# Performance work log

Hardware: AMD Instinct MI355X
Metric: run time of the kernel (lower is better)

The kernel has to match this reference:

```python
import jax, jax.numpy as jnp
import numpy as np

N_EMBD = 768
N_HEAD = 12
B, T = 2, 2048


def setup_inputs() -> dict:
    key = jax.random.key(0)
    ks = jax.random.split(key, 8)
    C = N_EMBD
    s = 0.02
    return {
        "x": jax.random.normal(ks[0], (B, T, C), jnp.float32),
        "ln1_g": jnp.ones((C,), jnp.float32),
        "ln1_b": jnp.zeros((C,), jnp.float32),
        "w_attn": jax.random.normal(ks[1], (C, 3 * C), jnp.float32) * s,
        "b_attn": jnp.zeros((3 * C,), jnp.float32),
        "w_attn_proj": jax.random.normal(ks[2], (C, C), jnp.float32) * s,
        "b_attn_proj": jnp.zeros((C,), jnp.float32),
        "ln2_g": jnp.ones((C,), jnp.float32),
        "ln2_b": jnp.zeros((C,), jnp.float32),
        "w_fc": jax.random.normal(ks[3], (C, 4 * C), jnp.float32) * s,
        "b_fc": jnp.zeros((4 * C,), jnp.float32),
        "w_mlp_proj": jax.random.normal(ks[4], (4 * C, C), jnp.float32) * s,
        "b_mlp_proj": jnp.zeros((C,), jnp.float32),
    }


def _layernorm(x, g, b, eps=1e-5):
    mu = jnp.mean(x, axis=-1, keepdims=True)
    var = jnp.mean(jnp.square(x - mu), axis=-1, keepdims=True)
    return (x - mu) * jax.lax.rsqrt(var + eps) * g + b


def _new_gelu(x):
    c = np.sqrt(2.0 / np.pi).astype(np.float32)
    return 0.5 * x * (1.0 + jnp.tanh(c * (x + 0.044715 * x * x * x)))


def _block(x, ln1_g, ln1_b, w_attn, b_attn, w_attn_proj, b_attn_proj,
           ln2_g, ln2_b, w_fc, b_fc, w_mlp_proj, b_mlp_proj):
    Bx, Tx, C = x.shape
    hd = C // N_HEAD
    h = _layernorm(x, ln1_g, ln1_b)
    qkv = h @ w_attn + b_attn  # [B,T,3C]
    q, k, v = jnp.split(qkv, 3, axis=-1)
    # [B,H,T,hd]
    q = q.reshape(Bx, Tx, N_HEAD, hd).transpose(0, 2, 1, 3)
    k = k.reshape(Bx, Tx, N_HEAD, hd).transpose(0, 2, 1, 3)
    v = v.reshape(Bx, Tx, N_HEAD, hd).transpose(0, 2, 1, 3)
    att = jnp.einsum('bhqd,bhkd->bhqk', q, k) * (1.0 / np.sqrt(hd))
    causal = jnp.tril(jnp.ones((Tx, Tx), bool))
    att = jnp.where(causal[None, None], att, -jnp.inf)
    att = jax.nn.softmax(att, axis=-1)
    y = jnp.einsum('bhqk,bhkd->bhqd', att, v)
    y = y.transpose(0, 2, 1, 3).reshape(Bx, Tx, C)
    x = x + y @ w_attn_proj + b_attn_proj
    h2 = _layernorm(x, ln2_g, ln2_b)
    x = x + _new_gelu(h2 @ w_fc + b_fc) @ w_mlp_proj + b_mlp_proj
    return x


def reference(x, ln1_g, ln1_b, w_attn, b_attn, w_attn_proj, b_attn_proj,
              ln2_g, ln2_b, w_fc, b_fc, w_mlp_proj, b_mlp_proj):
    return _block(x, ln1_g, ln1_b, w_attn, b_attn, w_attn_proj, b_attn_proj,
                  ln2_g, ln2_b, w_fc, b_fc, w_mlp_proj, b_mlp_proj)
```

## Files before the change

### kernel.cpp

```cpp
#include <hip/hip_runtime.h>
#include <hip/hip_bf16.h>
#include <math.h>

#define N_EMBD 768
#define N_HEAD 12
#define BATCH  2
#define SEQ    2048
#define ROWS   (BATCH*SEQ)
#define C3     (3*N_EMBD)

typedef __bf16 bf16;
typedef __attribute__((ext_vector_type(8))) __bf16 bf16x8;
typedef __attribute__((ext_vector_type(4))) float f32x4;

__device__ __forceinline__ void async16(const bf16* g, bf16* l) {
    __builtin_amdgcn_global_load_lds(
        (const __attribute__((address_space(1))) uint32_t*)g,
        (__attribute__((address_space(3))) uint32_t*)l, 16, 0, 0);
}

__global__ __launch_bounds__(256) void k_transpose_all(
    const float* __restrict__ w0, bf16* __restrict__ o0,
    const float* __restrict__ w1, bf16* __restrict__ o1,
    const float* __restrict__ w2, bf16* __restrict__ o2,
    const float* __restrict__ w3, bf16* __restrict__ o3)
{
    __shared__ bf16 tile[32][33];
    int bid = blockIdx.x;
    const float* in; bf16* out; int K, N, local;
    if      (bid < 1728) { in = w0; out = o0; K = 768;  N = 2304; local = bid; }
    else if (bid < 2304) { in = w1; out = o1; K = 768;  N = 768;  local = bid - 1728; }
    else if (bid < 4608) { in = w2; out = o2; K = 768;  N = 3072; local = bid - 2304; }
    else                 { in = w3; out = o3; K = 3072; N = 768;  local = bid - 4608; }
    int nt = N / 32;
    int n0 = (local % nt) * 32, k0 = (local / nt) * 32;
    int tc = threadIdx.x & 31, tr = threadIdx.x >> 5;
    #pragma unroll
    for (int i = 0; i < 4; i++) {
        int r = tr + i * 8;
        tile[r][tc] = (bf16)in[(size_t)(k0 + r) * N + n0 + tc];
    }
    __syncthreads();
    #pragma unroll
    for (int i = 0; i < 4; i++) {
        int r = tr + i * 8;
        out[(size_t)(n0 + r) * K + k0 + tc] = tile[tc][r];
    }
}

__global__ __launch_bounds__(256) void k_vtrans(
    const bf16* __restrict__ qkv, bf16* __restrict__ vt)
{
    __shared__ bf16 tile[32][33];
    int tt = blockIdx.x;
    int bh = blockIdx.y;
    int dt = blockIdx.z;
    int b = bh / N_HEAD, h = bh % N_HEAD;
    int tc = threadIdx.x & 31, tr = threadIdx.x >> 5;
    #pragma unroll
    for (int i = 0; i < 4; i++) {
        int r = tr + i * 8;
        tile[r][tc] = qkv[(size_t)(b * SEQ + tt * 32 + r) * C3 + 2 * N_EMBD + h * 64 + dt * 32 + tc];
    }
    __syncthreads();
    #pragma unroll
    for (int i = 0; i < 4; i++) {
        int r = tr + i * 8;
        vt[(size_t)(bh * 64 + dt * 32 + r) * SEQ + tt * 32 + tc] = tile[tc][r];
    }
}

__global__ __launch_bounds__(256) void k_layernorm(
    const float* __restrict__ x, const float* __restrict__ g,
    const float* __restrict__ b, bf16* __restrict__ out)
{
    int wave = threadIdx.x >> 6, lane = threadIdx.x & 63;
    int row = blockIdx.x * 4 + wave;
    const float4* xr = (const float4*)(x + (size_t)row * N_EMBD);
    const float4* g4 = (const float4*)g;
    const float4* b4 = (const float4*)b;
    float4 v[3];
    float s = 0.f, sq = 0.f;
    #pragma unroll
    for (int i = 0; i < 3; i++) {
        v[i] = xr[lane + 64 * i];
        s  += v[i].x + v[i].y + v[i].z + v[i].w;
        sq += v[i].x * v[i].x + v[i].y * v[i].y + v[i].z * v[i].z + v[i].w * v[i].w;
    }
    #pragma unroll
    for (int off = 32; off > 0; off >>= 1) {
        s  += __shfl_xor(s, off);
        sq += __shfl_xor(sq, off);
    }
    float mu  = s * (1.f / N_EMBD);
    float var = sq * (1.f / N_EMBD) - mu * mu;
    float rs  = rsqrtf(var + 1e-5f);
    bf16* orow = out + (size_t)row * N_EMBD;
    #pragma unroll
    for (int i = 0; i < 3; i++) {
        float4 gv = g4[lane + 64 * i], bv = b4[lane + 64 * i];
        union { ushort4 u4; bf16 e[4]; } pk;
        pk.e[0] = (bf16)((v[i].x - mu) * rs * gv.x + bv.x);
        pk.e[1] = (bf16)((v[i].y - mu) * rs * gv.y + bv.y);
        pk.e[2] = (bf16)((v[i].z - mu) * rs * gv.z + bv.z);
        pk.e[3] = (bf16)((v[i].w - mu) * rs * gv.w + bv.w);
        *(ushort4*)&orow[(lane + 64 * i) * 4] = pk.u4;
    }
}

template<int BN, int ACT, bool RES, bool OUT_BF16>
__global__ __launch_bounds__(256) void k_gemm(
    const bf16* __restrict__ A, const bf16* __restrict__ Bt,
    const float* __restrict__ bias, const float* __restrict__ res,
    void* __restrict__ outp, int M, int N, int K)
{
    constexpr int WC  = BN / 64;
    constexpr int WR  = 4 / WC;
    constexpr int RPW = 128 / WR;
    constexpr int MI  = RPW / 16;
    __shared__ __align__(16) bf16 As[128 * 32];
    __shared__ __align__(16) bf16 Bs[BN * 32];
    int n0 = blockIdx.x * BN, m0 = blockIdx.y * 128;
    int t = threadIdx.x;
    int lane = t & 63, wave = t >> 6;
    int wr = wave / WC, wc = wave % WC;
    int quad = lane >> 4, l16 = lane & 15;

    f32x4 acc[MI][4];
    #pragma unroll
    for (int i = 0; i < MI; i++)
        #pragma unroll
        for (int j = 0; j < 4; j++) acc[i][j] = (f32x4){0.f, 0.f, 0.f, 0.f};

    int sr = t >> 2;
    int sc = t & 3;
    int gsw = ((sc ^ ((sr ^ (sr >> 2)) & 3))) * 8;
    int rsw = (quad ^ ((l16 ^ (l16 >> 2)) & 3)) * 8;

    for (int k0 = 0; k0 < K; k0 += 32) {
        __syncthreads();
        #pragma unroll
        for (int p = 0; p < 2; p++) {
            int r = sr + p * 64;
            async16(&A[(size_t)(m0 + r) * K + k0 + gsw], &As[r * 32 + sc * 8]);
        }
        #pragma unroll
        for (int p = 0; p < BN / 64; p++) {
            int r = sr + p * 64;
            async16(&Bt[(size_t)(n0 + r) * K + k0 + gsw], &Bs[r * 32 + sc * 8]);
        }
        __syncthreads();
        bf16x8 af[MI], bfv[4];
        #pragma unroll
        for (int i = 0; i < MI; i++)
            af[i]  = *(bf16x8*)&As[(wr * RPW + i * 16 + l16) * 32 + rsw];
        #pragma unroll
        for (int j = 0; j < 4; j++)
            bfv[j] = *(bf16x8*)&Bs[(wc * 64 + j * 16 + l16) * 32 + rsw];
        #pragma unroll
        for (int i = 0; i < MI; i++)
            #pragma unroll
            for (int j = 0; j < 4; j++)
                acc[i][j] = __builtin_amdgcn_mfma_f32_16x16x32_bf16(af[i], bfv[j], acc[i][j], 0, 0, 0);
    }

    float* outf = (float*)outp;
    bf16*  outb = (bf16*)outp;
    #pragma unroll
    for (int i = 0; i < MI; i++) {
        #pragma unroll
        for (int j = 0; j < 4; j++) {
            int col = n0 + wc * 64 + j * 16 + l16;
            float bv = bias[col];
            #pragma unroll
            for (int r = 0; r < 4; r++) {
                int row = m0 + wr * RPW + i * 16 + quad * 4 + r;
                float v = acc[i][j][r] + bv;
                if (ACT == 1) {
                    float z = 0.7978845608f * (v + 0.044715f * v * v * v);
                    v = v / (1.f + __expf(-2.f * z));
                }
                if (RES) v += res[(size_t)row * N + col];
                if (OUT_BF16) outb[(size_t)row * N + col] = (bf16)v;
                else          outf[(size_t)row * N + col] = v;
            }
        }
    }
}

#define PS_S 72
__global__ __launch_bounds__(256) void k_flash(
    const bf16* __restrict__ qkv, const bf16* __restrict__ vt, bf16* __restrict__ y)
{
    __shared__ __align__(16) bf16 Ks[2][64 * 64];
    __shared__ __align__(16) bf16 VTl[2][64 * 64];
    __shared__ __align__(16) bf16 Ps[4][16 * PS_S];
    int bid = blockIdx.x;
    int hi = bid >> 8;
    int lo = bid & 255;
    int g  = lo >> 3;
    int e  = lo & 7;
    int bh = hi * 8 + e;
    int qt;
    if      (hi == 0) qt = g;
    else if (hi == 1) qt = (g + 16) & 31;
    else              qt = (g < 16) ? (30 - 2 * g) : (63 - 2 * g);
    int b = bh / N_HEAD, h = bh % N_HEAD;
    int t = threadIdx.x, lane = t & 63, wave = t >> 6;
    int quad = lane >> 4, l16 = lane & 15;
    int qbase = qt * 64 + wave * 16;

    bf16x8 qa[2];
    {
        const bf16* qrow = qkv + (size_t)(b * SEQ + qbase + l16) * C3 + h * 64;
        #pragma unroll
        for (int kh = 0; kh < 2; kh++) {
            union { uint4 u4; bf16 e8[8]; bf16x8 vv; } uq;
            uq.u4 = *(const uint4*)&qrow[quad * 8 + kh * 32];
            #pragma unroll
            for (int j = 0; j < 8; j++) uq.e8[j] = (bf16)((float)uq.e8[j] * 0.125f);
            qa[kh] = uq.vv;
        }
    }
    float l_part[4] = {0.f, 0.f, 0.f, 0.f};
    f32x4 o[4];
    #pragma unroll
    for (int j = 0; j < 4; j++) o[j] = (f32x4){0.f, 0.f, 0.f, 0.f};

    int sr = t >> 3;
    int sc = t & 7;
    int gsw = (sc ^ (sr & 7)) * 8;

    const bf16* kg = qkv + (size_t)b * SEQ * C3 + N_EMBD + h * 64;
    const bf16* vg = vt + (size_t)bh * 64 * SEQ;

    auto stage = [&](int tile, int bufi) {
        int k0 = tile * 64;
        #pragma unroll
        for (int p = 0; p < 2; p++) {
            int rr = sr + 32 * p;
            async16(&kg[(size_t)(k0 + rr) * C3 + gsw],  &Ks[bufi][rr * 64 + sc * 8]);
            async16(&vg[(size_t)rr * SEQ + k0 + gsw], &VTl[bufi][rr * 64 + sc * 8]);
        }
    };

    int ntiles = qt + 1;
    stage(0, 0);

    for (int tt = 0; tt < ntiles; tt++) {
        int bufi = tt & 1;
        int k0 = tt * 64;
        __syncthreads();
        if (tt + 1 < ntiles) stage(tt + 1, bufi ^ 1);

        f32x4 s[4];
        #pragma unroll
        for (int nt = 0; nt < 4; nt++) {
            bf16x8 b0 = *(bf16x8*)&Ks[bufi][(nt * 16 + l16) * 64 + (((quad    ) ^ (l16 & 7)) * 8)];
            bf16x8 b1 = *(bf16x8*)&Ks[bufi][(nt * 16 + l16) * 64 + (((quad + 4) ^ (l16 & 7)) * 8)];
            f32x4 z = (f32x4){0.f, 0.f, 0.f, 0.f};
            z = __builtin_amdgcn_mfma_f32_16x16x32_bf16(qa[0], b0, z, 0, 0, 0);
            z = __builtin_amdgcn_mfma_f32_16x16x32_bf16(qa[1], b1, z, 0, 0, 0);
            s[nt] = z;
        }
        bool diag = (tt == qt);
        float p[4][4];
        #pragma unroll
        for (int nt = 0; nt < 4; nt++) {
            int key = k0 + nt * 16 + l16;
            #pragma unroll
            for (int r = 0; r < 4; r++) {
                float pv = __expf(s[nt][r]);
                if (diag && key > qbase + quad * 4 + r) pv = 0.f;
                p[nt][r] = pv;
                l_part[r] += pv;
            }
        }
        #pragma unroll
        for (int nt = 0; nt < 4; nt++)
            #pragma unroll
            for (int r = 0; r < 4; r++)
                Ps[wave][(quad * 4 + r) * PS_S + nt * 16 + l16] = (bf16)p[nt][r];
        bf16x8 pa[2];
        #pragma unroll
        for (int kt = 0; kt < 2; kt++)
            pa[kt] = *(bf16x8*)&Ps[wave][l16 * PS_S + kt * 32 + quad * 8];
        #pragma unroll
        for (int jt = 0; jt < 4; jt++) {
            int d = jt * 16 + l16;
            #pragma unroll
            for (int kt = 0; kt < 2; kt++) {
                bf16x8 vb = *(bf16x8*)&VTl[bufi][d * 64 + (((quad + 4 * kt) ^ (l16 & 7)) * 8)];
                o[jt] = __builtin_amdgcn_mfma_f32_16x16x32_bf16(pa[kt], vb, o[jt], 0, 0, 0);
            }
        }
    }
    #pragma unroll
    for (int r = 0; r < 4; r++) {
        #pragma unroll
        for (int off = 8; off > 0; off >>= 1) l_part[r] += __shfl_xor(l_part[r], off);
    }
    #pragma unroll
    for (int jt = 0; jt < 4; jt++)
        #pragma unroll
        for (int r = 0; r < 4; r++) {
            int q = qbase + quad * 4 + r;
            y[(size_t)(b * SEQ + q) * N_EMBD + h * 64 + jt * 16 + l16] =
                (bf16)(o[jt][r] / l_part[r]);
        }
}

extern "C" void kernel_launch(void* const* d_in, const int* in_sizes, int n_in,
                              void* d_out, int out_size, void* d_ws, size_t ws_size,
                              hipStream_t stream) {
    const float* x           = (const float*)d_in[0];
    const float* ln1_g       = (const float*)d_in[1];
    const float* ln1_b       = (const float*)d_in[2];
    const float* w_attn      = (const float*)d_in[3];
    const float* b_attn      = (const float*)d_in[4];
    const float* w_attn_proj = (const float*)d_in[5];
    const float* b_attn_proj = (const float*)d_in[6];
    const float* ln2_g       = (const float*)d_in[7];
    const float* ln2_b       = (const float*)d_in[8];
    const float* w_fc        = (const float*)d_in[9];
    const float* b_fc        = (const float*)d_in[10];
    const float* w_mlp_proj  = (const float*)d_in[11];
    const float* b_mlp_proj  = (const float*)d_in[12];

    char* ws = (char*)d_ws;
    size_t off = 0;
    auto alloc = [&](size_t n) -> void* {
        off = (off + 255) & ~(size_t)255;
        void* p = ws + off;
        off += n;
        return p;
    };
    bf16* wqkvT  = (bf16*)alloc((size_t)C3 * N_EMBD * 2);
    bf16* wprojT = (bf16*)alloc((size_t)N_EMBD * N_EMBD * 2);
    bf16* wfcT   = (bf16*)alloc((size_t)4 * N_EMBD * N_EMBD * 2);
    bf16* wmlpT  = (bf16*)alloc((size_t)N_EMBD * 4 * N_EMBD * 2);
    bf16* hbuf   = (bf16*)alloc((size_t)ROWS * N_EMBD * 2);
    float* x2    = (float*)alloc((size_t)ROWS * N_EMBD * 4);
    bf16* yb     = (bf16*)alloc((size_t)ROWS * N_EMBD * 2);
    bf16* vtb    = (bf16*)alloc((size_t)BATCH * N_HEAD * 64 * SEQ * 2);
    bf16* big    = (bf16*)alloc((size_t)ROWS * 4 * N_EMBD * 2);
    bf16* qkvb   = big;
    bf16* actb   = big;

    k_transpose_all<<<6912, 256, 0, stream>>>(w_attn, wqkvT, w_attn_proj, wprojT,
                                              w_fc, wfcT, w_mlp_proj, wmlpT);

    k_layernorm<<<ROWS / 4, 256, 0, stream>>>(x, ln1_g, ln1_b, hbuf);
    k_gemm<128, 0, false, true ><<<dim3(C3 / 128,  ROWS / 128), 256, 0, stream>>>(
        hbuf, wqkvT,  b_attn,      nullptr, qkvb, ROWS, C3,     N_EMBD);
    k_vtrans<<<dim3(SEQ / 32, BATCH * N_HEAD, 2), 256, 0, stream>>>(qkvb, vtb);
    k_flash<<<768, 256, 0, stream>>>(qkvb, vtb, yb);
    k_gemm<64,  0, true,  false><<<dim3(N_EMBD / 64, ROWS / 128), 256, 0, stream>>>(
        yb,   wprojT, b_attn_proj, x,       x2,   ROWS, N_EMBD, N_EMBD);
    k_layernorm<<<ROWS / 4, 256, 0, stream>>>(x2, ln2_g, ln2_b, hbuf);
    k_gemm<128, 1, false, true ><<<dim3(3072 / 128, ROWS / 128), 256, 0, stream>>>(
        hbuf, wfcT,   b_fc,        nullptr, actb, ROWS, 3072,   N_EMBD);
    k_gemm<64,  0, true,  false><<<dim3(N_EMBD / 64, ROWS / 128), 256, 0, stream>>>(
        actb, wmlpT,  b_mlp_proj,  x2, (float*)d_out, ROWS, N_EMBD, 3072);
}
```

Baseline: 308.3 us.

## Deepen GEMM K-tile to 64, add LDS double buffering and M-major grid order

The GEMM K-step grows from 32 to 64 with a new XOR swizzle for the wider LDS rows. An optional double-buffered path prefetches the next K tile with async global-to-LDS loads while the current one is computed, which removes one barrier per iteration. A grid-swap option makes blockIdx.x walk M tiles so that concurrent blocks share B columns. The projection GEMMs get both options and the FC GEMM gets only the swap. The cost is more LDS per block, which may lower occupancy.

```diff
diff --git a/kernel.cpp b/kernel.cpp
--- a/kernel.cpp
+++ b/kernel.cpp
@@ -108,7 +108,7 @@
     }
 }
 
-template<int BN, int ACT, bool RES, bool OUT_BF16>
+template<int BN, int ACT, bool RES, bool OUT_BF16, bool MSWAP, bool DBUF>
 __global__ __launch_bounds__(256) void k_gemm(
     const bf16* __restrict__ A, const bf16* __restrict__ Bt,
     const float* __restrict__ bias, const float* __restrict__ res,
@@ -118,9 +118,11 @@
     constexpr int WR  = 4 / WC;
     constexpr int RPW = 128 / WR;
     constexpr int MI  = RPW / 16;
-    __shared__ __align__(16) bf16 As[128 * 32];
-    __shared__ __align__(16) bf16 Bs[BN * 32];
-    int n0 = blockIdx.x * BN, m0 = blockIdx.y * 128;
+    constexpr int NB  = DBUF ? 2 : 1;
+    __shared__ __align__(16) bf16 As[NB][128 * 64];
+    __shared__ __align__(16) bf16 Bs[NB][BN * 64];
+    int n0 = (MSWAP ? blockIdx.y : blockIdx.x) * BN;
+    int m0 = (MSWAP ? blockIdx.x : blockIdx.y) * 128;
     int t = threadIdx.x;
     int lane = t & 63, wave = t >> 6;
     int wr = wave / WC, wc = wave % WC;
@@ -132,36 +134,55 @@
         #pragma unroll
         for (int j = 0; j < 4; j++) acc[i][j] = (f32x4){0.f, 0.f, 0.f, 0.f};
 
-    int sr = t >> 2;
-    int sc = t & 3;
-    int gsw = ((sc ^ ((sr ^ (sr >> 2)) & 3))) * 8;
-    int rsw = (quad ^ ((l16 ^ (l16 >> 2)) & 3)) * 8;
-
-    for (int k0 = 0; k0 < K; k0 += 32) {
-        __syncthreads();
-        #pragma unroll
-        for (int p = 0; p < 2; p++) {
-            int r = sr + p * 64;
-            async16(&A[(size_t)(m0 + r) * K + k0 + gsw], &As[r * 32 + sc * 8]);
-        }
-        #pragma unroll
-        for (int p = 0; p < BN / 64; p++) {
-            int r = sr + p * 64;
-            async16(&Bt[(size_t)(n0 + r) * K + k0 + gsw], &Bs[r * 32 + sc * 8]);
-        }
-        __syncthreads();
-        bf16x8 af[MI], bfv[4];
-        #pragma unroll
-        for (int i = 0; i < MI; i++)
-            af[i]  = *(bf16x8*)&As[(wr * RPW + i * 16 + l16) * 32 + rsw];
-        #pragma unroll
-        for (int j = 0; j < 4; j++)
-            bfv[j] = *(bf16x8*)&Bs[(wc * 64 + j * 16 + l16) * 32 + rsw];
-        #pragma unroll
-        for (int i = 0; i < MI; i++)
+    int sr = t >> 3;
+    int sc = t & 7;
+    int gsw = (sc ^ (sr & 7)) * 8;
+
+    auto stage = [&](int k0, int bi) {
+        #pragma unroll
+        for (int p = 0; p < 4; p++) {
+            int r = sr + p * 32;
+            async16(&A[(size_t)(m0 + r) * K + k0 + gsw], &As[bi][r * 64 + sc * 8]);
+        }
+        #pragma unroll
+        for (int p = 0; p < BN / 32; p++) {
+            int r = sr + p * 32;
+            async16(&Bt[(size_t)(n0 + r) * K + k0 + gsw], &Bs[bi][r * 64 + sc * 8]);
+        }
+    };
+    auto compute = [&](int bi) {
+        #pragma unroll
+        for (int kh = 0; kh < 2; kh++) {
+            bf16x8 af[MI], bfv[4];
+            #pragma unroll
+            for (int i = 0; i < MI; i++)
+                af[i]  = *(bf16x8*)&As[bi][(wr * RPW + i * 16 + l16) * 64 + (((quad + 4 * kh) ^ (l16 & 7)) * 8)];
             #pragma unroll
             for (int j = 0; j < 4; j++)
-                acc[i][j] = __builtin_amdgcn_mfma_f32_16x16x32_bf16(af[i], bfv[j], acc[i][j], 0, 0, 0);
+                bfv[j] = *(bf16x8*)&Bs[bi][(wc * 64 + j * 16 + l16) * 64 + (((quad + 4 * kh) ^ (l16 & 7)) * 8)];
+            #pragma unroll
+            for (int i = 0; i < MI; i++)
+                #pragma unroll
+                for (int j = 0; j < 4; j++)
+                    acc[i][j] = __builtin_amdgcn_mfma_f32_16x16x32_bf16(af[i], bfv[j], acc[i][j], 0, 0, 0);
+        }
+    };
+
+    if (DBUF) {
+        stage(0, 0);
+        int bi = 0;
+        for (int k0 = 0; k0 < K; k0 += 64, bi ^= 1) {
+            __syncthreads();
+            if (k0 + 64 < K) stage(k0 + 64, bi ^ 1);
+            compute(bi);
+        }
+    } else {
+        for (int k0 = 0; k0 < K; k0 += 64) {
+            __syncthreads();
+            stage(k0, 0);
+            __syncthreads();
+            compute(0);
+        }
     }
 
     float* outf = (float*)outp;
@@ -351,15 +372,15 @@
                                               w_fc, wfcT, w_mlp_proj, wmlpT);
 
     k_layernorm<<<ROWS / 4, 256, 0, stream>>>(x, ln1_g, ln1_b, hbuf);
-    k_gemm<128, 0, false, true ><<<dim3(C3 / 128,  ROWS / 128), 256, 0, stream>>>(
+    k_gemm<128, 0, false, true,  false, false><<<dim3(C3 / 128, ROWS / 128), 256, 0, stream>>>(
         hbuf, wqkvT,  b_attn,      nullptr, qkvb, ROWS, C3,     N_EMBD);
     k_vtrans<<<dim3(SEQ / 32, BATCH * N_HEAD, 2), 256, 0, stream>>>(qkvb, vtb);
     k_flash<<<768, 256, 0, stream>>>(qkvb, vtb, yb);
-    k_gemm<64,  0, true,  false><<<dim3(N_EMBD / 64, ROWS / 128), 256, 0, stream>>>(
+    k_gemm<64,  0, true,  false, true,  true ><<<dim3(ROWS / 128, N_EMBD / 64), 256, 0, stream>>>(
         yb,   wprojT, b_attn_proj, x,       x2,   ROWS, N_EMBD, N_EMBD);
     k_layernorm<<<ROWS / 4, 256, 0, stream>>>(x2, ln2_g, ln2_b, hbuf);
-    k_gemm<128, 1, false, true ><<<dim3(3072 / 128, ROWS / 128), 256, 0, stream>>>(
+    k_gemm<128, 1, false, true,  true,  false><<<dim3(ROWS / 128, 3072 / 128), 256, 0, stream>>>(
         hbuf, wfcT,   b_fc,        nullptr, actb, ROWS, 3072,   N_EMBD);
-    k_gemm<64,  0, true,  false><<<dim3(N_EMBD / 64, ROWS / 128), 256, 0, stream>>>(
+    k_gemm<64,  0, true,  false, true,  true ><<<dim3(ROWS / 128, N_EMBD / 64), 256, 0, stream>>>(
         actb, wmlpT,  b_mlp_proj,  x2, (float*)d_out, ROWS, N_EMBD, 3072);
 }
```

Result: faster. 282.0 us (-8.5%).
